# Kernel optimization log

Measured on AMD Instinct MI355X. Metric: run time of the kernel, lower is better.

The kernel has to match this reference:

```python
import jax, jax.numpy as jnp
import numpy as np

B, N, K, M = 4, 32768, 128, 1024
C_IN, C_OUT, C_ATT, H = 256, 256, 256, 8
G = 32  # GroupNorm groups
EPS = 1e-6


def heat_diffusion(x, mass, evals, evecs, t):
    # to_basis: evecs^T @ (mass * x)  -> [B,K,C]
    x_spec = jnp.einsum('bnk,bnc->bkc', evecs, x * mass[..., None])
    coefs = jnp.exp(-evals[..., None] * t[None, None, :])  # [B,K,C]
    # from_basis: evecs @ spec -> [B,N,C]
    return jnp.einsum('bnk,bkc->bnc', evecs, coefs * x_spec)


def setup_inputs() -> dict:
    key = jax.random.key(0)
    ks = jax.random.split(key, 16)
    x = jax.random.normal(ks[0], (B, N, C_IN), jnp.float32)
    mass = jax.random.uniform(ks[1], (B, N), jnp.float32, 0.1, 1.0)
    evals = jnp.sort(jax.random.uniform(ks[2], (B, K), jnp.float32, 0.0, 10.0), axis=-1)
    evecs = jax.random.normal(ks[3], (B, N, K), jnp.float32) / np.sqrt(N)
    # unique sorted farthest-point indices per mesh (equiv. to boolean mask with M True)
    far_idx = jnp.stack([jnp.sort(jax.random.permutation(jax.random.fold_in(ks[4], b), N)[:M])
                         for b in range(B)]).astype(jnp.int32)
    s = 1.0 / np.sqrt(C_IN)
    params = dict(
        diff_in_t=jnp.full((C_IN,), 0.01, jnp.float32),
        diff_out_t=jnp.full((C_OUT,), 0.01, jnp.float32),
        gn_w=jnp.ones((C_IN,), jnp.float32),
        gn_b=jnp.zeros((C_IN,), jnp.float32),
        Wq=jax.random.normal(ks[5], (C_IN, C_ATT), jnp.float32) * s,
        bq=jnp.zeros((C_ATT,), jnp.float32),
        Wk=jax.random.normal(ks[6], (C_IN, C_ATT), jnp.float32) * s,
        bk=jnp.zeros((C_ATT,), jnp.float32),
        Wv=jax.random.normal(ks[7], (C_IN, C_ATT), jnp.float32) * s,
        bv=jnp.zeros((C_ATT,), jnp.float32),
        Wo=jax.random.normal(ks[8], (C_ATT, C_OUT), jnp.float32) * s,
        bo=jnp.zeros((C_OUT,), jnp.float32),
        out_w=jnp.ones((C_OUT,), jnp.float32),
    )
    return dict(x=x, mass=mass, evals=evals, evecs=evecs, far_idx=far_idx, **params)


def reference(x, mass, evals, evecs, far_idx, diff_in_t, diff_out_t, gn_w, gn_b,
              Wq, bq, Wk, bk, Wv, bv, Wo, bo, out_w):
    # clamp (torch does this in-place under no_grad)
    diff_in_t = jnp.maximum(diff_in_t, 1e-8)
    diff_out_t = jnp.maximum(diff_out_t, 1e-8)
    out_w = jnp.maximum(out_w, 1e-8)

    x = heat_diffusion(x, mass, evals, evecs, diff_in_t)  # [B,N,C_IN]

    # masked gather of farthest points -> [B,M,C_IN]
    x_far = jnp.take_along_axis(x, far_idx[..., None], axis=1)

    # GroupNorm over (group-channels, points)
    xg = x_far.reshape(B, M, G, C_IN // G)
    mu = jnp.mean(xg, axis=(1, 3), keepdims=True)
    var = jnp.var(xg, axis=(1, 3), keepdims=True)
    xg = (xg - mu) * jax.lax.rsqrt(var + EPS)
    x_far = xg.reshape(B, M, C_IN) * gn_w + gn_b

    d = C_ATT // H
    q = (x_far @ Wq + bq).reshape(B, M, H, d)
    k = (x_far @ Wk + bk).reshape(B, M, H, d)
    v = (x_far @ Wv + bv).reshape(B, M, H, d)
    scores = jnp.einsum('bqhd,bkhd->bhqk', q, k) / np.sqrt(d)
    attn = jax.nn.softmax(scores, axis=-1)
    x_far = jnp.einsum('bhqk,bkhd->bqhd', attn, v).reshape(B, M, C_ATT)
    x_far = x_far @ Wo + bo  # [B,M,C_OUT]

    # scatter back into zeros at the farthest-point rows
    z = jnp.zeros((B, N, C_OUT), x.dtype)
    z = z.at[jnp.arange(B)[:, None], far_idx].set(x_far)

    out = heat_diffusion(z, mass, evals, evecs, diff_out_t)
    return out * out_w[None, None, :]
```

## Files before the change

### kernel.cpp

```cpp
#include <hip/hip_runtime.h>
#include <hip/hip_bf16.h>


#define Bn 4
#define Nn 32768
#define Kn 128
#define Cn 256
#define Mn 1024
#define Hn 8
#define Dn 32
#define NCH 64
#define MCH 16
#define SEG 8

typedef _Float16 f16;
typedef _Float16 f16x8 __attribute__((ext_vector_type(8)));
typedef float f32x4 __attribute__((ext_vector_type(4)));

__device__ __forceinline__ void gload_lds16(const float* g, float* l) {
    __builtin_amdgcn_global_load_lds(
        (const __attribute__((address_space(1))) void*)g,
        (__attribute__((address_space(3))) void*)l, 16, 0, 0);
}

__global__ __launch_bounds__(512) void k_tobasis1(
    const float* __restrict__ x, const float* __restrict__ mass,
    const float* __restrict__ evecs, float* __restrict__ part)
{
    const int nch = blockIdx.x, b = blockIdx.z;
    const int n0 = nch * (Nn / NCH);
    const int t = threadIdx.x;
    const int lane = t & 63, w = t >> 6;
    const int lr = lane & 15, lg = lane >> 4;
    const int wm = (w & 1) * 64;
    const int wc = (w >> 1) * 64;

    __shared__ __align__(16) float evS[2][32][128];
    __shared__ __align__(16) float xS[2][32][256];
    __shared__ __align__(16) f16 evT[128][64];
    __shared__ __align__(16) f16 xT[256][64];
    __shared__ __align__(16) float massS[512];

    const size_t rb0 = (size_t)b * Nn + n0;
    const float* ebase = evecs + rb0 * Kn;
    const float* xbase = x + rb0 * Cn;

    f32x4 acc[4][4] = {};

    if (w < 2) gload_lds16(mass + rb0 + w * 256 + lane * 4, massS + w * 256);
#pragma unroll
    for (int ss = 0; ss < 2; ss++) {
        const float* eb = ebase + (size_t)ss * 32 * Kn;
        const float* xb = xbase + (size_t)ss * 32 * Cn;
#pragma unroll
        for (int iw = 0; iw < 2; iw++)
            gload_lds16(eb + (w * 2 + iw) * 256 + lane * 4, &evS[ss][0][0] + (w * 2 + iw) * 256);
#pragma unroll
        for (int iw = 0; iw < 4; iw++)
            gload_lds16(xb + (w * 4 + iw) * 256 + lane * 4, &xS[ss][0][0] + (w * 4 + iw) * 256);
    }

    for (int s = 0; s < 16; s++) {
        const int p = s & 1;
        if (s == 15) { asm volatile("s_waitcnt vmcnt(0)" ::: "memory"); }
        else         { asm volatile("s_waitcnt vmcnt(6)" ::: "memory"); }
        __builtin_amdgcn_sched_barrier(0);
        __builtin_amdgcn_s_barrier();

        {
            const int k = t & 127;
            const int g = t >> 7;
            f16x8 hv, lv;
#pragma unroll
            for (int r = 0; r < 8; r++) {
                const float f = evS[p][g * 8 + r][k];
                const f16 h = (f16)f;
                hv[r] = h;
                lv[r] = (f16)(f - (float)h);
            }
            *(f16x8*)&evT[k][((g) ^ (k & 7)) * 8] = hv;
            *(f16x8*)&evT[k][((4 + g) ^ (k & 7)) * 8] = lv;
        }
        {
            const int c = t & 255;
            const int g2 = t >> 8;
#pragma unroll
            for (int jj = 0; jj < 2; jj++) {
                const int ch = g2 * 2 + jj;
                f16x8 hv, lv;
#pragma unroll
                for (int r = 0; r < 8; r++) {
                    const int n = ch * 8 + r;
                    const float f = xS[p][n][c] * massS[s * 32 + n];
                    const f16 h = (f16)f;
                    hv[r] = h;
                    lv[r] = (f16)(f - (float)h);
                }
                *(f16x8*)&xT[c][((ch) ^ (c & 7)) * 8] = hv;
                *(f16x8*)&xT[c][((4 + ch) ^ (c & 7)) * 8] = lv;
            }
        }

        asm volatile("s_waitcnt lgkmcnt(0)" ::: "memory");
        __builtin_amdgcn_sched_barrier(0);
        __builtin_amdgcn_s_barrier();

        if (s + 2 < 16) {
            const float* eb = ebase + (size_t)(s + 2) * 32 * Kn;
            const float* xb = xbase + (size_t)(s + 2) * 32 * Cn;
#pragma unroll
            for (int iw = 0; iw < 2; iw++)
                gload_lds16(eb + (w * 2 + iw) * 256 + lane * 4, &evS[p][0][0] + (w * 2 + iw) * 256);
#pragma unroll
            for (int iw = 0; iw < 4; iw++)
                gload_lds16(xb + (w * 4 + iw) * 256 + lane * 4, &xS[p][0][0] + (w * 4 + iw) * 256);
        }

        f16x8 aH[4], aL[4], bH[4], bL[4];
#pragma unroll
        for (int i = 0; i < 4; i++) {
            const int rk = wm + i * 16 + lr;
            aH[i] = *(const f16x8*)&evT[rk][((lg) ^ (rk & 7)) * 8];
            aL[i] = *(const f16x8*)&evT[rk][((4 + lg) ^ (rk & 7)) * 8];
            const int rc = wc + i * 16 + lr;
            bH[i] = *(const f16x8*)&xT[rc][((lg) ^ (rc & 7)) * 8];
            bL[i] = *(const f16x8*)&xT[rc][((4 + lg) ^ (rc & 7)) * 8];
        }
#pragma unroll
        for (int i = 0; i < 4; i++)
#pragma unroll
            for (int j = 0; j < 4; j++) {
                acc[i][j] = __builtin_amdgcn_mfma_f32_16x16x32_f16(aH[i], bH[j], acc[i][j], 0, 0, 0);
                acc[i][j] = __builtin_amdgcn_mfma_f32_16x16x32_f16(aH[i], bL[j], acc[i][j], 0, 0, 0);
                acc[i][j] = __builtin_amdgcn_mfma_f32_16x16x32_f16(aL[i], bH[j], acc[i][j], 0, 0, 0);
            }
    }

    float* dst = part + ((size_t)b * NCH + nch) * (Kn * Cn);
#pragma unroll
    for (int i = 0; i < 4; i++)
#pragma unroll
        for (int j = 0; j < 4; j++) {
            const int m0 = wm + i * 16 + lg * 4;
            const int c = wc + j * 16 + lr;
#pragma unroll
            for (int r = 0; r < 4; r++)
                dst[(size_t)(m0 + r) * Cn + c] = acc[i][j][r];
        }
}

__global__ __launch_bounds__(256) void k_reduce(
    const float* __restrict__ part, int nchunks,
    const float* __restrict__ evals, const float* __restrict__ tvec,
    float* __restrict__ spec)
{
    const int b = blockIdx.x >> 7, k = blockIdx.x & 127, c = threadIdx.x;
    float ssum = 0.f;
    const float* p = part + ((size_t)b * nchunks * Kn + k) * Cn + c;
    for (int j = 0; j < nchunks; j++) ssum += p[(size_t)j * Kn * Cn];
    const float lam = evals[b * Kn + k];
    const float tt = fmaxf(tvec[c], 1e-8f);
    spec[((size_t)b * Kn + k) * Cn + c] = ssum * __expf(-lam * tt);
}

__global__ __launch_bounds__(128) void k_gather(
    const float* __restrict__ evecs, const float* __restrict__ mass,
    const int* __restrict__ far, float* __restrict__ evf, float* __restrict__ massf)
{
    const int row = blockIdx.x;
    const int b = row >> 10;
    const int idx = far[row];
    const int t = threadIdx.x;
    evf[(size_t)row * Kn + t] = evecs[((size_t)b * Nn + idx) * Kn + t];
    if (t == 0) massf[row] = mass[(size_t)b * Nn + idx];
}

struct G3 {
    const float* W[3];
    const float* bias[3];
    float* out[3];
};

template<int KD, bool PERB, bool MMASS>
__global__ __launch_bounds__(256) void k_gemm64(
    const float* __restrict__ X, G3 g, const float* __restrict__ massf)
{
    const int mt = blockIdx.x, ct = blockIdx.y, z = blockIdx.z;
    const int row0 = mt * 64, c0 = ct * 64;
    const int b = row0 >> 10;
    const float* Wp = g.W[z];
    const float* bias = g.bias[z];
    float* out = g.out[z];
    const size_t woff = PERB ? (size_t)b * KD * 256 : 0;

    __shared__ float xT[32][68];
    __shared__ float wl[32][64];
    const int t = threadIdx.x, tx = t & 15, ty = t >> 4;
    float acc[4][4] = {};

    for (int k0 = 0; k0 < KD; k0 += 32) {
        {
            const int m = t >> 2, cc0 = (t & 3) * 8;
            const float* xs = X + (size_t)(row0 + m) * KD + k0 + cc0;
            float4 a0 = *(const float4*)xs, a1 = *(const float4*)(xs + 4);
            xT[cc0 + 0][m] = a0.x; xT[cc0 + 1][m] = a0.y; xT[cc0 + 2][m] = a0.z; xT[cc0 + 3][m] = a0.w;
            xT[cc0 + 4][m] = a1.x; xT[cc0 + 5][m] = a1.y; xT[cc0 + 6][m] = a1.z; xT[cc0 + 7][m] = a1.w;
        }
        {
            const int cc = t >> 3, col = (t & 7) * 8;
            const float* wsrc = Wp + woff + (size_t)(k0 + cc) * 256 + c0 + col;
            float4 a0 = *(const float4*)wsrc, a1 = *(const float4*)(wsrc + 4);
            wl[cc][col + 0] = a0.x; wl[cc][col + 1] = a0.y; wl[cc][col + 2] = a0.z; wl[cc][col + 3] = a0.w;
            wl[cc][col + 4] = a1.x; wl[cc][col + 5] = a1.y; wl[cc][col + 6] = a1.z; wl[cc][col + 7] = a1.w;
        }
        __syncthreads();
#pragma unroll 8
        for (int cc = 0; cc < 32; cc++) {
            float4 xv = *(const float4*)&xT[cc][ty * 4];
            float4 wv = *(const float4*)&wl[cc][tx * 4];
            float xa[4] = {xv.x, xv.y, xv.z, xv.w};
            float wa[4] = {wv.x, wv.y, wv.z, wv.w};
#pragma unroll
            for (int i = 0; i < 4; i++)
#pragma unroll
                for (int j = 0; j < 4; j++) acc[i][j] += xa[i] * wa[j];
        }
        __syncthreads();
    }
    float bj[4] = {0.f, 0.f, 0.f, 0.f};
    if (bias) {
#pragma unroll
        for (int j = 0; j < 4; j++) bj[j] = bias[c0 + tx * 4 + j];
    }
#pragma unroll
    for (int i = 0; i < 4; i++) {
        const int row = row0 + ty * 4 + i;
        const float mm = MMASS ? massf[row] : 1.f;
        *(float4*)(out + (size_t)row * 256 + c0 + tx * 4) =
            make_float4((acc[i][0] + bj[0]) * mm, (acc[i][1] + bj[1]) * mm,
                        (acc[i][2] + bj[2]) * mm, (acc[i][3] + bj[3]) * mm);
    }
}

__global__ __launch_bounds__(256) void k_gnstats(const float* __restrict__ xfar, float* __restrict__ gst)
{
    const int b = blockIdx.x >> 5, g = blockIdx.x & 31;
    const int t = threadIdx.x;
    float s = 0.f, s2 = 0.f;
#pragma unroll
    for (int i = 0; i < 4; i++) {
        const int m = t * 4 + i;
        const float* p = xfar + ((size_t)b * Mn + m) * Cn + g * 8;
        float4 a = *(const float4*)p;
        float4 c = *(const float4*)(p + 4);
        s += a.x + a.y + a.z + a.w + c.x + c.y + c.z + c.w;
        s2 += a.x * a.x + a.y * a.y + a.z * a.z + a.w * a.w +
              c.x * c.x + c.y * c.y + c.z * c.z + c.w * c.w;
    }
    __shared__ float sb[256], sb2[256];
    sb[t] = s; sb2[t] = s2;
    __syncthreads();
    for (int o = 128; o > 0; o >>= 1) {
        if (t < o) { sb[t] += sb[t + o]; sb2[t] += sb2[t + o]; }
        __syncthreads();
    }
    if (t == 0) {
        const float mean = sb[0] * (1.f / 8192.f);
        const float var = sb2[0] * (1.f / 8192.f) - mean * mean;
        gst[2 * blockIdx.x] = mean;
        gst[2 * blockIdx.x + 1] = rsqrtf(var + 1e-6f);
    }
}

__global__ __launch_bounds__(256) void k_gnapply(
    const float* __restrict__ xfar, const float* __restrict__ gst,
    const float* __restrict__ gw, const float* __restrict__ gb, float* __restrict__ xn)
{
    const int idx = (blockIdx.x * 256 + threadIdx.x) * 4;
    const int c = idx & 255;
    const int row = idx >> 8;
    const int b = row >> 10;
    const int g = c >> 3;
    const float2 st = *(const float2*)&gst[2 * (b * 32 + g)];
    float4 vv = *(const float4*)&xfar[idx];
    float4 w4 = *(const float4*)&gw[c];
    float4 b4 = *(const float4*)&gb[c];
    float4 o;
    o.x = (vv.x - st.x) * st.y * w4.x + b4.x;
    o.y = (vv.y - st.x) * st.y * w4.y + b4.y;
    o.z = (vv.z - st.x) * st.y * w4.z + b4.z;
    o.w = (vv.w - st.x) * st.y * w4.w + b4.w;
    *(float4*)&xn[idx] = o;
}

__global__ __launch_bounds__(256) void k_attn(
    const float* __restrict__ q, const float* __restrict__ kbuf, const float* __restrict__ vbuf,
    float* __restrict__ pacc, float* __restrict__ pm, float* __restrict__ pl)
{
    const int qt = blockIdx.x;
    const int seg = blockIdx.y;
    const int bh = blockIdx.z;
    const int b = bh >> 3, h = bh & 7;
    const int t = threadIdx.x;
    const int tx = t & 15, ty = t >> 4;

    __shared__ float qT[32][68];
    __shared__ float kT[32][68];
    __shared__ float vsm[64][36];
    __shared__ float psT[64][72];
    __shared__ float red[64][16];

    const int q0 = qt * 64;
    {
        const int row = t >> 2, d0 = (t & 3) * 8;
        const float* qp = q + ((size_t)b * Mn + q0 + row) * Cn + h * Dn + d0;
        float4 a0 = *(const float4*)qp, a1 = *(const float4*)(qp + 4);
        qT[d0 + 0][row] = a0.x; qT[d0 + 1][row] = a0.y; qT[d0 + 2][row] = a0.z; qT[d0 + 3][row] = a0.w;
        qT[d0 + 4][row] = a1.x; qT[d0 + 5][row] = a1.y; qT[d0 + 6][row] = a1.z; qT[d0 + 7][row] = a1.w;
    }

    const float scale = 0.17677669529663687f;
    float m_i[4], l_i[4], acc[4][2];
#pragma unroll
    for (int i = 0; i < 4; i++) { m_i[i] = -1e30f; l_i[i] = 0.f; acc[i][0] = 0.f; acc[i][1] = 0.f; }

    for (int kt = 0; kt < 2; kt++) {
        __syncthreads();
        {
            const int row = t >> 2, d0 = (t & 3) * 8;
            const int k0 = seg * 128 + kt * 64;
            const float* kp = kbuf + ((size_t)b * Mn + k0 + row) * Cn + h * Dn + d0;
            float4 a0 = *(const float4*)kp, a1 = *(const float4*)(kp + 4);
            kT[d0 + 0][row] = a0.x; kT[d0 + 1][row] = a0.y; kT[d0 + 2][row] = a0.z; kT[d0 + 3][row] = a0.w;
            kT[d0 + 4][row] = a1.x; kT[d0 + 5][row] = a1.y; kT[d0 + 6][row] = a1.z; kT[d0 + 7][row] = a1.w;
            const float* vp = vbuf + ((size_t)b * Mn + k0 + row) * Cn + h * Dn + d0;
            *(float4*)&vsm[row][d0] = *(const float4*)vp;
            *(float4*)&vsm[row][d0 + 4] = *(const float4*)(vp + 4);
        }
        __syncthreads();

        float s[4][4] = {};
#pragma unroll 8
        for (int d = 0; d < 32; d++) {
            float4 qv = *(const float4*)&qT[d][ty * 4];
            float4 kv = *(const float4*)&kT[d][tx * 4];
            float qa[4] = {qv.x, qv.y, qv.z, qv.w};
            float ka[4] = {kv.x, kv.y, kv.z, kv.w};
#pragma unroll
            for (int i = 0; i < 4; i++)
#pragma unroll
                for (int j = 0; j < 4; j++) s[i][j] += qa[i] * ka[j];
        }
        float tmax[4];
#pragma unroll
        for (int i = 0; i < 4; i++) {
            s[i][0] *= scale; s[i][1] *= scale; s[i][2] *= scale; s[i][3] *= scale;
            tmax[i] = fmaxf(fmaxf(s[i][0], s[i][1]), fmaxf(s[i][2], s[i][3]));
        }
#pragma unroll
        for (int i = 0; i < 4; i++) red[ty * 4 + i][tx] = tmax[i];
        __syncthreads();
        float nm[4];
#pragma unroll
        for (int i = 0; i < 4; i++) {
            const int row = ty * 4 + i;
            float mx = m_i[i];
#pragma unroll
            for (int xj = 0; xj < 16; xj++) mx = fmaxf(mx, red[row][xj]);
            nm[i] = mx;
        }
        __syncthreads();
        float tsum[4];
#pragma unroll
        for (int i = 0; i < 4; i++) {
            float p0 = __expf(s[i][0] - nm[i]);
            float p1 = __expf(s[i][1] - nm[i]);
            float p2 = __expf(s[i][2] - nm[i]);
            float p3 = __expf(s[i][3] - nm[i]);
            s[i][0] = p0; s[i][1] = p1; s[i][2] = p2; s[i][3] = p3;
            tsum[i] = p0 + p1 + p2 + p3;
        }
#pragma unroll
        for (int kk = 0; kk < 4; kk++)
            *(float4*)&psT[tx * 4 + kk][ty * 4] = make_float4(s[0][kk], s[1][kk], s[2][kk], s[3][kk]);
#pragma unroll
        for (int i = 0; i < 4; i++) red[ty * 4 + i][tx] = tsum[i];
        __syncthreads();
#pragma unroll
        for (int i = 0; i < 4; i++) {
            const int row = ty * 4 + i;
            float rs = 0.f;
#pragma unroll
            for (int xj = 0; xj < 16; xj++) rs += red[row][xj];
            const float r = __expf(m_i[i] - nm[i]);
            l_i[i] = l_i[i] * r + rs;
            m_i[i] = nm[i];
            acc[i][0] *= r; acc[i][1] *= r;
        }
#pragma unroll 8
        for (int k = 0; k < 64; k++) {
            float4 pv = *(const float4*)&psT[k][ty * 4];
            float2 vv = *(const float2*)&vsm[k][tx * 2];
            acc[0][0] += pv.x * vv.x; acc[0][1] += pv.x * vv.y;
            acc[1][0] += pv.y * vv.x; acc[1][1] += pv.y * vv.y;
            acc[2][0] += pv.z * vv.x; acc[2][1] += pv.z * vv.y;
            acc[3][0] += pv.w * vv.x; acc[3][1] += pv.w * vv.y;
        }
    }
#pragma unroll
    for (int i = 0; i < 4; i++) {
        const int m = q0 + ty * 4 + i;
        const size_t pr = (((size_t)seg * Bn + b) * Hn + h) * Mn + m;
        if (tx == 0) { pm[pr] = m_i[i]; pl[pr] = l_i[i]; }
        *(float2*)(pacc + pr * 32 + tx * 2) = make_float2(acc[i][0], acc[i][1]);
    }
}

__global__ __launch_bounds__(256) void k_comb(
    const float* __restrict__ pacc, const float* __restrict__ pm, const float* __restrict__ pl,
    float* __restrict__ att)
{
    const int t = threadIdx.x;
    const size_t row = (size_t)blockIdx.x * 8 + (t >> 5);
    const int j = t & 31;
    float M = -1e30f;
#pragma unroll
    for (int s = 0; s < SEG; s++) M = fmaxf(M, pm[(size_t)s * 32768 + row]);
    float L = 0.f, a = 0.f;
#pragma unroll
    for (int s = 0; s < SEG; s++) {
        const float w = __expf(pm[(size_t)s * 32768 + row] - M);
        L += w * pl[(size_t)s * 32768 + row];
        a += w * pacc[((size_t)s * 32768 + row) * 32 + j];
    }
    const int bh = (int)(row >> 10);
    const int mrow = (int)(row & 1023);
    const int b = bh >> 3, h = bh & 7;
    att[((size_t)b * Mn + mrow) * Cn + h * 32 + j] = a / L;
}

__global__ __launch_bounds__(256) void k_tobasis2(
    const float* __restrict__ evf, const float* __restrict__ xo, float* __restrict__ part)
{
    const int mch = blockIdx.x, ct = blockIdx.y, b = blockIdx.z;
    const int m0 = mch * (Mn / MCH);
    const int c0 = ct * 128;
    __shared__ float ev[32][128];
    __shared__ float xm[32][128];
    const int t = threadIdx.x, tx = t & 15, ty = t >> 4;
    float acc[8][8];
#pragma unroll
    for (int i = 0; i < 8; i++)
#pragma unroll
        for (int j = 0; j < 8; j++) acc[i][j] = 0.f;
    const int lr = t >> 3, lc = (t & 7) * 16;
    for (int s = 0; s < Mn / MCH; s += 32) {
        const size_t mrow = (size_t)b * Mn + m0 + s + lr;
        {
            const float* es = evf + mrow * Kn + lc;
            *(float4*)&ev[lr][lc]      = *(const float4*)es;
            *(float4*)&ev[lr][lc + 4]  = *(const float4*)(es + 4);
            *(float4*)&ev[lr][lc + 8]  = *(const float4*)(es + 8);
            *(float4*)&ev[lr][lc + 12] = *(const float4*)(es + 12);
            const float* xs = xo + mrow * Cn + c0 + lc;
            *(float4*)&xm[lr][lc]      = *(const float4*)xs;
            *(float4*)&xm[lr][lc + 4]  = *(const float4*)(xs + 4);
            *(float4*)&xm[lr][lc + 8]  = *(const float4*)(xs + 8);
            *(float4*)&xm[lr][lc + 12] = *(const float4*)(xs + 12);
        }
        __syncthreads();
#pragma unroll 4
        for (int nn = 0; nn < 32; nn++) {
            float4 e0 = *(const float4*)&ev[nn][ty * 4];
            float4 e1 = *(const float4*)&ev[nn][64 + ty * 4];
            float4 x0 = *(const float4*)&xm[nn][tx * 4];
            float4 x1 = *(const float4*)&xm[nn][64 + tx * 4];
            float ee[8] = {e0.x, e0.y, e0.z, e0.w, e1.x, e1.y, e1.z, e1.w};
            float xx[8] = {x0.x, x0.y, x0.z, x0.w, x1.x, x1.y, x1.z, x1.w};
#pragma unroll
            for (int i = 0; i < 8; i++)
#pragma unroll
                for (int j = 0; j < 8; j++) acc[i][j] += ee[i] * xx[j];
        }
        __syncthreads();
    }
    float* dst = part + ((size_t)b * MCH + mch) * (Kn * Cn);
#pragma unroll
    for (int i = 0; i < 8; i++) {
        const int k = (i < 4) ? (ty * 4 + i) : (64 + ty * 4 + i - 4);
        *(float4*)(dst + (size_t)k * Cn + c0 + tx * 4) =
            make_float4(acc[i][0], acc[i][1], acc[i][2], acc[i][3]);
        *(float4*)(dst + (size_t)k * Cn + c0 + 64 + tx * 4) =
            make_float4(acc[i][4], acc[i][5], acc[i][6], acc[i][7]);
    }
}

__global__ __launch_bounds__(256) void k_frombasis2(
    const float* __restrict__ evecs, const float* __restrict__ spec,
    const float* __restrict__ outw, float* __restrict__ out)
{
    const int nt = blockIdx.x, ct = blockIdx.y, b = blockIdx.z;
    const int n0 = nt * 128, c0 = ct * 128;
    __shared__ float evT[32][132];
    __shared__ float sp[32][128];
    const int t = threadIdx.x, tx = t & 15, ty = t >> 4;
    float acc[8][8];
#pragma unroll
    for (int i = 0; i < 8; i++)
#pragma unroll
        for (int j = 0; j < 8; j++) acc[i][j] = 0.f;
    const int en = t >> 1, ek0 = (t & 1) * 16;
    const int sr = t >> 3, sc = (t & 7) * 16;
    for (int k0 = 0; k0 < Kn; k0 += 32) {
        {
            const float* es = evecs + ((size_t)b * Nn + n0 + en) * Kn + k0 + ek0;
            float4 a0 = *(const float4*)es, a1 = *(const float4*)(es + 4);
            float4 a2 = *(const float4*)(es + 8), a3 = *(const float4*)(es + 12);
            evT[ek0 + 0][en] = a0.x; evT[ek0 + 1][en] = a0.y; evT[ek0 + 2][en] = a0.z; evT[ek0 + 3][en] = a0.w;
            evT[ek0 + 4][en] = a1.x; evT[ek0 + 5][en] = a1.y; evT[ek0 + 6][en] = a1.z; evT[ek0 + 7][en] = a1.w;
            evT[ek0 + 8][en] = a2.x; evT[ek0 + 9][en] = a2.y; evT[ek0 + 10][en] = a2.z; evT[ek0 + 11][en] = a2.w;
            evT[ek0 + 12][en] = a3.x; evT[ek0 + 13][en] = a3.y; evT[ek0 + 14][en] = a3.z; evT[ek0 + 15][en] = a3.w;
            const float* ss = spec + ((size_t)b * Kn + k0 + sr) * Cn + c0 + sc;
            *(float4*)&sp[sr][sc]      = *(const float4*)ss;
            *(float4*)&sp[sr][sc + 4]  = *(const float4*)(ss + 4);
            *(float4*)&sp[sr][sc + 8]  = *(const float4*)(ss + 8);
            *(float4*)&sp[sr][sc + 12] = *(const float4*)(ss + 12);
        }
        __syncthreads();
#pragma unroll 4
        for (int kk2 = 0; kk2 < 32; kk2++) {
            float4 e0 = *(const float4*)&evT[kk2][ty * 4];
            float4 e1 = *(const float4*)&evT[kk2][64 + ty * 4];
            float4 s0 = *(const float4*)&sp[kk2][tx * 4];
            float4 s1 = *(const float4*)&sp[kk2][64 + tx * 4];
            float ee[8] = {e0.x, e0.y, e0.z, e0.w, e1.x, e1.y, e1.z, e1.w};
            float sv[8] = {s0.x, s0.y, s0.z, s0.w, s1.x, s1.y, s1.z, s1.w};
#pragma unroll
            for (int i = 0; i < 8; i++)
#pragma unroll
                for (int j = 0; j < 8; j++) acc[i][j] += ee[i] * sv[j];
        }
        __syncthreads();
    }
    float ow[8];
#pragma unroll
    for (int j = 0; j < 8; j++) {
        const int c = c0 + ((j < 4) ? (tx * 4 + j) : (64 + tx * 4 + j - 4));
        ow[j] = fmaxf(outw[c], 1e-8f);
    }
#pragma unroll
    for (int i = 0; i < 8; i++) {
        const int n = n0 + ((i < 4) ? (ty * 4 + i) : (64 + ty * 4 + i - 4));
        float* od = out + ((size_t)b * Nn + n) * Cn + c0;
        *(float4*)(od + tx * 4) =
            make_float4(acc[i][0] * ow[0], acc[i][1] * ow[1], acc[i][2] * ow[2], acc[i][3] * ow[3]);
        *(float4*)(od + 64 + tx * 4) =
            make_float4(acc[i][4] * ow[4], acc[i][5] * ow[5], acc[i][6] * ow[6], acc[i][7] * ow[7]);
    }
}

extern "C" void kernel_launch(void* const* d_in, const int* in_sizes, int n_in,
                              void* d_out, int out_size, void* d_ws, size_t ws_size,
                              hipStream_t stream)
{
    const float* x     = (const float*)d_in[0];
    const float* mass  = (const float*)d_in[1];
    const float* evals = (const float*)d_in[2];
    const float* evecs = (const float*)d_in[3];
    const int*   far   = (const int*)d_in[4];
    const float* t_in  = (const float*)d_in[5];
    const float* t_out = (const float*)d_in[6];
    const float* gn_w  = (const float*)d_in[7];
    const float* gn_b  = (const float*)d_in[8];
    const float* Wq    = (const float*)d_in[9];
    const float* bq    = (const float*)d_in[10];
    const float* Wk    = (const float*)d_in[11];
    const float* bk    = (const float*)d_in[12];
    const float* Wv    = (const float*)d_in[13];
    const float* bv    = (const float*)d_in[14];
    const float* Wo    = (const float*)d_in[15];
    const float* bo    = (const float*)d_in[16];
    const float* outw  = (const float*)d_in[17];
    float* out = (float*)d_out;
    float* ws = (float*)d_ws;

    float* A     = ws;
    float* evf   = ws    + 8388608;
    float* massf = evf   + 524288;
    float* gst   = massf + 4096;
    float* pm    = gst   + 256;
    float* pl    = pm    + 262144;
    float* spec1 = pl    + 262144;
    float* xfar  = spec1 + 131072;
    float* xn    = xfar  + 1048576;
    float* q     = xn    + 1048576;
    float* kk    = q     + 1048576;
    float* v     = kk    + 1048576;
    float* pacc  = A;
    float* part2 = A;
    float* spec2 = spec1;
    float* xo    = xfar;
    float* att   = xn;

    k_tobasis1<<<dim3(NCH, 1, Bn), 512, 0, stream>>>(x, mass, evecs, A);
    k_reduce<<<Bn * Kn, Cn, 0, stream>>>(A, NCH, evals, t_in, spec1);
    k_gather<<<Bn * Mn, Kn, 0, stream>>>(evecs, mass, far, evf, massf);
    {
        G3 g{};
        g.W[0] = spec1; g.bias[0] = nullptr; g.out[0] = xfar;
        k_gemm64<128, true, false><<<dim3(64, 4, 1), 256, 0, stream>>>(evf, g, nullptr);
    }
    k_gnstats<<<Bn * 32, 256, 0, stream>>>(xfar, gst);
    k_gnapply<<<1024, 256, 0, stream>>>(xfar, gst, gn_w, gn_b, xn);
    {
        G3 g{};
        g.W[0] = Wq; g.W[1] = Wk; g.W[2] = Wv;
        g.bias[0] = bq; g.bias[1] = bk; g.bias[2] = bv;
        g.out[0] = q; g.out[1] = kk; g.out[2] = v;
        k_gemm64<256, false, false><<<dim3(64, 4, 3), 256, 0, stream>>>(xn, g, nullptr);
    }
    k_attn<<<dim3(16, SEG, 32), 256, 0, stream>>>(q, kk, v, pacc, pm, pl);
    k_comb<<<4096, 256, 0, stream>>>(pacc, pm, pl, att);
    {
        G3 g{};
        g.W[0] = Wo; g.bias[0] = bo; g.out[0] = xo;
        k_gemm64<256, false, true><<<dim3(64, 4, 1), 256, 0, stream>>>(att, g, massf);
    }
    k_tobasis2<<<dim3(MCH, 2, Bn), 256, 0, stream>>>(evf, xo, part2);
    k_reduce<<<Bn * Kn, Cn, 0, stream>>>(part2, MCH, evals, t_out, spec2);
    k_frombasis2<<<dim3(256, 2, Bn), 256, 0, stream>>>(evecs, spec2, outw, out);
}
```

Baseline: 600.7 us.

## Rewrite attention as MFMA flash kernel with split-f16 precision, drop combine pass

The scalar FP32 split-KV attention kernel and its separate combine kernel are replaced by one flash-attention kernel per (query tile, batch-head). It uses 16x16x32 f16 MFMA with hi/lo f16 splitting (three MFMAs per product) to keep near-FP32 accuracy. It also prefetches the next K/V tile into registers and uses wave shuffles for the row max and sum. This removes the partial-result writes and the combine launch, but the grid is eight times smaller (512 blocks) and each block now loops over all 16 key tiles.

```diff
diff --git a/kernel.cpp b/kernel.cpp
--- a/kernel.cpp
+++ b/kernel.cpp
@@ -11,16 +11,23 @@
 #define Dn 32
 #define NCH 64
 #define MCH 16
-#define SEG 8
 
 typedef _Float16 f16;
 typedef _Float16 f16x8 __attribute__((ext_vector_type(8)));
 typedef float f32x4 __attribute__((ext_vector_type(4)));
+typedef unsigned int u32;
+typedef unsigned int u32x4 __attribute__((ext_vector_type(4)));
 
 __device__ __forceinline__ void gload_lds16(const float* g, float* l) {
     __builtin_amdgcn_global_load_lds(
         (const __attribute__((address_space(1))) void*)g,
         (__attribute__((address_space(3))) void*)l, 16, 0, 0);
+}
+
+static __device__ __forceinline__ u32 packf16(f16 a, f16 b) {
+    union { f16 h[2]; u32 u; } x;
+    x.h[0] = a; x.h[1] = b;
+    return x.u;
 }
 
 __global__ __launch_bounds__(512) void k_tobasis1(
@@ -295,148 +302,196 @@
 
 __global__ __launch_bounds__(256) void k_attn(
     const float* __restrict__ q, const float* __restrict__ kbuf, const float* __restrict__ vbuf,
-    float* __restrict__ pacc, float* __restrict__ pm, float* __restrict__ pl)
+    float* __restrict__ att)
 {
     const int qt = blockIdx.x;
-    const int seg = blockIdx.y;
-    const int bh = blockIdx.z;
+    const int bh = blockIdx.y;
     const int b = bh >> 3, h = bh & 7;
     const int t = threadIdx.x;
-    const int tx = t & 15, ty = t >> 4;
-
-    __shared__ float qT[32][68];
-    __shared__ float kT[32][68];
-    __shared__ float vsm[64][36];
-    __shared__ float psT[64][72];
-    __shared__ float red[64][16];
-
+    const int lane = t & 63, w = t >> 6;
+    const int lr = lane & 15, lg = lane >> 4;
+
+    __shared__ __align__(16) f16 Kh[64][32];
+    __shared__ __align__(16) f16 Kl[64][32];
+    __shared__ __align__(16) f16 Vh[32][64];
+    __shared__ __align__(16) f16 Vl[32][64];
+    __shared__ __align__(16) u32 Pw[4][16][68];
+
+    const size_t base = (size_t)b * Mn * Cn + h * Dn;
     const int q0 = qt * 64;
+
+    f16x8 Qh, Ql;
     {
-        const int row = t >> 2, d0 = (t & 3) * 8;
-        const float* qp = q + ((size_t)b * Mn + q0 + row) * Cn + h * Dn + d0;
-        float4 a0 = *(const float4*)qp, a1 = *(const float4*)(qp + 4);
-        qT[d0 + 0][row] = a0.x; qT[d0 + 1][row] = a0.y; qT[d0 + 2][row] = a0.z; qT[d0 + 3][row] = a0.w;
-        qT[d0 + 4][row] = a1.x; qT[d0 + 5][row] = a1.y; qT[d0 + 6][row] = a1.z; qT[d0 + 7][row] = a1.w;
-    }
-
-    const float scale = 0.17677669529663687f;
-    float m_i[4], l_i[4], acc[4][2];
-#pragma unroll
-    for (int i = 0; i < 4; i++) { m_i[i] = -1e30f; l_i[i] = 0.f; acc[i][0] = 0.f; acc[i][1] = 0.f; }
-
-    for (int kt = 0; kt < 2; kt++) {
-        __syncthreads();
-        {
-            const int row = t >> 2, d0 = (t & 3) * 8;
-            const int k0 = seg * 128 + kt * 64;
-            const float* kp = kbuf + ((size_t)b * Mn + k0 + row) * Cn + h * Dn + d0;
-            float4 a0 = *(const float4*)kp, a1 = *(const float4*)(kp + 4);
-            kT[d0 + 0][row] = a0.x; kT[d0 + 1][row] = a0.y; kT[d0 + 2][row] = a0.z; kT[d0 + 3][row] = a0.w;
-            kT[d0 + 4][row] = a1.x; kT[d0 + 5][row] = a1.y; kT[d0 + 6][row] = a1.z; kT[d0 + 7][row] = a1.w;
-            const float* vp = vbuf + ((size_t)b * Mn + k0 + row) * Cn + h * Dn + d0;
-            *(float4*)&vsm[row][d0] = *(const float4*)vp;
-            *(float4*)&vsm[row][d0 + 4] = *(const float4*)(vp + 4);
-        }
-        __syncthreads();
-
-        float s[4][4] = {};
-#pragma unroll 8
-        for (int d = 0; d < 32; d++) {
-            float4 qv = *(const float4*)&qT[d][ty * 4];
-            float4 kv = *(const float4*)&kT[d][tx * 4];
-            float qa[4] = {qv.x, qv.y, qv.z, qv.w};
-            float ka[4] = {kv.x, kv.y, kv.z, kv.w};
-#pragma unroll
-            for (int i = 0; i < 4; i++)
-#pragma unroll
-                for (int j = 0; j < 4; j++) s[i][j] += qa[i] * ka[j];
-        }
-        float tmax[4];
-#pragma unroll
-        for (int i = 0; i < 4; i++) {
-            s[i][0] *= scale; s[i][1] *= scale; s[i][2] *= scale; s[i][3] *= scale;
-            tmax[i] = fmaxf(fmaxf(s[i][0], s[i][1]), fmaxf(s[i][2], s[i][3]));
-        }
-#pragma unroll
-        for (int i = 0; i < 4; i++) red[ty * 4 + i][tx] = tmax[i];
-        __syncthreads();
-        float nm[4];
-#pragma unroll
-        for (int i = 0; i < 4; i++) {
-            const int row = ty * 4 + i;
-            float mx = m_i[i];
-#pragma unroll
-            for (int xj = 0; xj < 16; xj++) mx = fmaxf(mx, red[row][xj]);
-            nm[i] = mx;
-        }
-        __syncthreads();
-        float tsum[4];
-#pragma unroll
-        for (int i = 0; i < 4; i++) {
-            float p0 = __expf(s[i][0] - nm[i]);
-            float p1 = __expf(s[i][1] - nm[i]);
-            float p2 = __expf(s[i][2] - nm[i]);
-            float p3 = __expf(s[i][3] - nm[i]);
-            s[i][0] = p0; s[i][1] = p1; s[i][2] = p2; s[i][3] = p3;
-            tsum[i] = p0 + p1 + p2 + p3;
-        }
-#pragma unroll
-        for (int kk = 0; kk < 4; kk++)
-            *(float4*)&psT[tx * 4 + kk][ty * 4] = make_float4(s[0][kk], s[1][kk], s[2][kk], s[3][kk]);
-#pragma unroll
-        for (int i = 0; i < 4; i++) red[ty * 4 + i][tx] = tsum[i];
-        __syncthreads();
-#pragma unroll
-        for (int i = 0; i < 4; i++) {
-            const int row = ty * 4 + i;
-            float rs = 0.f;
-#pragma unroll
-            for (int xj = 0; xj < 16; xj++) rs += red[row][xj];
-            const float r = __expf(m_i[i] - nm[i]);
-            l_i[i] = l_i[i] * r + rs;
-            m_i[i] = nm[i];
-            acc[i][0] *= r; acc[i][1] *= r;
-        }
-#pragma unroll 8
-        for (int k = 0; k < 64; k++) {
-            float4 pv = *(const float4*)&psT[k][ty * 4];
-            float2 vv = *(const float2*)&vsm[k][tx * 2];
-            acc[0][0] += pv.x * vv.x; acc[0][1] += pv.x * vv.y;
-            acc[1][0] += pv.y * vv.x; acc[1][1] += pv.y * vv.y;
-            acc[2][0] += pv.z * vv.x; acc[2][1] += pv.z * vv.y;
-            acc[3][0] += pv.w * vv.x; acc[3][1] += pv.w * vv.y;
-        }
-    }
-#pragma unroll
-    for (int i = 0; i < 4; i++) {
-        const int m = q0 + ty * 4 + i;
-        const size_t pr = (((size_t)seg * Bn + b) * Hn + h) * Mn + m;
-        if (tx == 0) { pm[pr] = m_i[i]; pl[pr] = l_i[i]; }
-        *(float2*)(pacc + pr * 32 + tx * 2) = make_float2(acc[i][0], acc[i][1]);
-    }
-}
-
-__global__ __launch_bounds__(256) void k_comb(
-    const float* __restrict__ pacc, const float* __restrict__ pm, const float* __restrict__ pl,
-    float* __restrict__ att)
-{
-    const int t = threadIdx.x;
-    const size_t row = (size_t)blockIdx.x * 8 + (t >> 5);
-    const int j = t & 31;
-    float M = -1e30f;
-#pragma unroll
-    for (int s = 0; s < SEG; s++) M = fmaxf(M, pm[(size_t)s * 32768 + row]);
-    float L = 0.f, a = 0.f;
-#pragma unroll
-    for (int s = 0; s < SEG; s++) {
-        const float w = __expf(pm[(size_t)s * 32768 + row] - M);
-        L += w * pl[(size_t)s * 32768 + row];
-        a += w * pacc[((size_t)s * 32768 + row) * 32 + j];
-    }
-    const int bh = (int)(row >> 10);
-    const int mrow = (int)(row & 1023);
-    const int b = bh >> 3, h = bh & 7;
-    att[((size_t)b * Mn + mrow) * Cn + h * 32 + j] = a / L;
+        const float* qp = q + base + (size_t)(q0 + w * 16 + lr) * Cn + lg * 8;
+        f32x4 a0 = *(const f32x4*)qp;
+        f32x4 a1 = *(const f32x4*)(qp + 4);
+        const float scale = 0.17677669529663687f;
+        float qv[8] = {a0[0], a0[1], a0[2], a0[3], a1[0], a1[1], a1[2], a1[3]};
+#pragma unroll
+        for (int r = 0; r < 8; r++) {
+            const float f = qv[r] * scale;
+            const f16 hh = (f16)f;
+            Qh[r] = hh;
+            Ql[r] = (f16)(f - (float)hh);
+        }
+    }
+
+    const int krow = t >> 2, kdg = (t & 3) * 8;
+    const int vrow = (t & 31) * 2, vdc = (t >> 5) * 4;
+
+    f32x4 kr0, kr1, va, vb;
+    {
+        const float* kp = kbuf + base + (size_t)krow * Cn + kdg;
+        kr0 = *(const f32x4*)kp; kr1 = *(const f32x4*)(kp + 4);
+        const float* vp = vbuf + base + (size_t)vrow * Cn + vdc;
+        va = *(const f32x4*)vp; vb = *(const f32x4*)(vp + Cn);
+    }
+
+    float m_i[4], l_i[4];
+    f32x4 acc[2] = {};
+#pragma unroll
+    for (int r = 0; r < 4; r++) { m_i[r] = -1e30f; l_i[r] = 0.f; }
+
+#pragma unroll 1
+    for (int kt = 0; kt < 16; kt++) {
+        asm volatile("" ::: "memory");
+        __builtin_amdgcn_s_barrier();
+
+        {
+            float kv[8] = {kr0[0], kr0[1], kr0[2], kr0[3], kr1[0], kr1[1], kr1[2], kr1[3]};
+            f16x8 hv, lv;
+#pragma unroll
+            for (int r = 0; r < 8; r++) {
+                const f16 hh = (f16)kv[r];
+                hv[r] = hh;
+                lv[r] = (f16)(kv[r] - (float)hh);
+            }
+            *(f16x8*)&Kh[krow][kdg] = hv;
+            *(f16x8*)&Kl[krow][kdg] = lv;
+        }
+        {
+            float v0[4] = {va[0], va[1], va[2], va[3]};
+            float v1[4] = {vb[0], vb[1], vb[2], vb[3]};
+#pragma unroll
+            for (int j = 0; j < 4; j++) {
+                const int d = vdc + j;
+                const f16 h0 = (f16)v0[j], h1 = (f16)v1[j];
+                const f16 l0 = (f16)(v0[j] - (float)h0), l1 = (f16)(v1[j] - (float)h1);
+                const int col = vrow >> 1;
+                const int idx = (((col >> 2) ^ (d & 7)) << 2) | (col & 3);
+                ((u32*)&Vh[d][0])[idx] = packf16(h0, h1);
+                ((u32*)&Vl[d][0])[idx] = packf16(l0, l1);
+            }
+        }
+        if (kt < 15) {
+            const float* kp = kbuf + base + (size_t)((kt + 1) * 64 + krow) * Cn + kdg;
+            kr0 = *(const f32x4*)kp; kr1 = *(const f32x4*)(kp + 4);
+            const float* vp = vbuf + base + (size_t)((kt + 1) * 64 + vrow) * Cn + vdc;
+            va = *(const f32x4*)vp; vb = *(const f32x4*)(vp + Cn);
+        }
+
+        asm volatile("s_waitcnt lgkmcnt(0)" ::: "memory");
+        __builtin_amdgcn_sched_barrier(0);
+        __builtin_amdgcn_s_barrier();
+
+        f32x4 s[4];
+#pragma unroll
+        for (int ct = 0; ct < 4; ct++) {
+            const f16x8 khi = *(const f16x8*)&Kh[ct * 16 + lr][lg * 8];
+            const f16x8 klo = *(const f16x8*)&Kl[ct * 16 + lr][lg * 8];
+            f32x4 z = {};
+            z = __builtin_amdgcn_mfma_f32_16x16x32_f16(Qh, khi, z, 0, 0, 0);
+            z = __builtin_amdgcn_mfma_f32_16x16x32_f16(Qh, klo, z, 0, 0, 0);
+            z = __builtin_amdgcn_mfma_f32_16x16x32_f16(Ql, khi, z, 0, 0, 0);
+            s[ct] = z;
+        }
+
+        float tm[4];
+#pragma unroll
+        for (int r = 0; r < 4; r++)
+            tm[r] = fmaxf(fmaxf(s[0][r], s[1][r]), fmaxf(s[2][r], s[3][r]));
+#pragma unroll
+        for (int r = 0; r < 4; r++) {
+            tm[r] = fmaxf(tm[r], __shfl_xor(tm[r], 1));
+            tm[r] = fmaxf(tm[r], __shfl_xor(tm[r], 2));
+            tm[r] = fmaxf(tm[r], __shfl_xor(tm[r], 4));
+            tm[r] = fmaxf(tm[r], __shfl_xor(tm[r], 8));
+        }
+        float corr[4], rs[4];
+#pragma unroll
+        for (int r = 0; r < 4; r++) {
+            const float nm = fmaxf(m_i[r], tm[r]);
+            corr[r] = __expf(m_i[r] - nm);
+            m_i[r] = nm;
+            rs[r] = 0.f;
+        }
+#pragma unroll
+        for (int ct = 0; ct < 4; ct++)
+#pragma unroll
+            for (int r = 0; r < 4; r++) {
+                const float p = __expf(s[ct][r] - m_i[r]);
+                rs[r] += p;
+                const f16 ph = (f16)p;
+                const f16 pl = (f16)(p - (float)ph);
+                Pw[w][lg * 4 + r][ct * 16 + lr] = packf16(ph, pl);
+            }
+#pragma unroll
+        for (int r = 0; r < 4; r++) {
+            rs[r] += __shfl_xor(rs[r], 1);
+            rs[r] += __shfl_xor(rs[r], 2);
+            rs[r] += __shfl_xor(rs[r], 4);
+            rs[r] += __shfl_xor(rs[r], 8);
+            l_i[r] = l_i[r] * corr[r] + rs[r];
+        }
+#pragma unroll
+        for (int dt = 0; dt < 2; dt++)
+#pragma unroll
+            for (int r = 0; r < 4; r++) acc[dt][r] *= corr[r];
+
+        asm volatile("s_waitcnt lgkmcnt(0)" ::: "memory");
+        __builtin_amdgcn_sched_barrier(0);
+
+        f16x8 pah[2], pal[2];
+#pragma unroll
+        for (int kc = 0; kc < 2; kc++) {
+            const u32* prow = &Pw[w][lr][0] + kc * 32 + lg * 8;
+            u32x4 ua = *(const u32x4*)prow;
+            u32x4 ub = *(const u32x4*)(prow + 4);
+            union { u32 wd[4]; f16x8 v; } hh, ll;
+            hh.wd[0] = __builtin_amdgcn_perm(ua[1], ua[0], 0x05040100u);
+            hh.wd[1] = __builtin_amdgcn_perm(ua[3], ua[2], 0x05040100u);
+            hh.wd[2] = __builtin_amdgcn_perm(ub[1], ub[0], 0x05040100u);
+            hh.wd[3] = __builtin_amdgcn_perm(ub[3], ub[2], 0x05040100u);
+            ll.wd[0] = __builtin_amdgcn_perm(ua[1], ua[0], 0x07060302u);
+            ll.wd[1] = __builtin_amdgcn_perm(ua[3], ua[2], 0x07060302u);
+            ll.wd[2] = __builtin_amdgcn_perm(ub[1], ub[0], 0x07060302u);
+            ll.wd[3] = __builtin_amdgcn_perm(ub[3], ub[2], 0x07060302u);
+            pah[kc] = hh.v;
+            pal[kc] = ll.v;
+        }
+
+#pragma unroll
+        for (int dt = 0; dt < 2; dt++)
+#pragma unroll
+            for (int kc = 0; kc < 2; kc++) {
+                const int d = dt * 16 + lr;
+                const int ch = ((kc * 4 + lg) ^ (lr & 7)) * 8;
+                const f16x8 vh = *(const f16x8*)&Vh[d][ch];
+                const f16x8 vl = *(const f16x8*)&Vl[d][ch];
+                acc[dt] = __builtin_amdgcn_mfma_f32_16x16x32_f16(pah[kc], vh, acc[dt], 0, 0, 0);
+                acc[dt] = __builtin_amdgcn_mfma_f32_16x16x32_f16(pah[kc], vl, acc[dt], 0, 0, 0);
+                acc[dt] = __builtin_amdgcn_mfma_f32_16x16x32_f16(pal[kc], vh, acc[dt], 0, 0, 0);
+            }
+    }
+
+#pragma unroll
+    for (int r = 0; r < 4; r++) {
+        const float inv = 1.f / l_i[r];
+        const size_t orow = (size_t)b * Mn + q0 + w * 16 + lg * 4 + r;
+#pragma unroll
+        for (int dt = 0; dt < 2; dt++)
+            att[orow * Cn + h * Dn + dt * 16 + lr] = acc[dt][r] * inv;
+    }
 }
 
 __global__ __launch_bounds__(256) void k_tobasis2(
@@ -596,11 +651,11 @@
     float* q     = xn    + 1048576;
     float* kk    = q     + 1048576;
     float* v     = kk    + 1048576;
-    float* pacc  = A;
     float* part2 = A;
     float* spec2 = spec1;
     float* xo    = xfar;
     float* att   = xn;
+    (void)pm; (void)pl;
 
     k_tobasis1<<<dim3(NCH, 1, Bn), 512, 0, stream>>>(x, mass, evecs, A);
     k_reduce<<<Bn * Kn, Cn, 0, stream>>>(A, NCH, evals, t_in, spec1);
@@ -619,8 +674,7 @@
         g.out[0] = q; g.out[1] = kk; g.out[2] = v;
         k_gemm64<256, false, false><<<dim3(64, 4, 3), 256, 0, stream>>>(xn, g, nullptr);
     }
-    k_attn<<<dim3(16, SEG, 32), 256, 0, stream>>>(q, kk, v, pacc, pm, pl);
-    k_comb<<<4096, 256, 0, stream>>>(pacc, pm, pl, att);
+    k_attn<<<dim3(16, 32), 256, 0, stream>>>(q, kk, v, att);
     {
         G3 g{};
         g.W[0] = Wo; g.bias[0] = bo; g.out[0] = xo;
```

Result: faster. 534.9 us (-11.0%).
